# Optimization experiments

Measured on AMD Instinct MI355X. Metric: run time of the kernel, lower is better.

Reference implementation:

```python
import jax, jax.numpy as jnp
import numpy as np

MAX_REL = 127  # default max_relative_position of NEZHA-style RelativePositionsEncoding


def rel_pos_encoding(L, d):
    """Clipped relative-distance sinusoidal encoding, shape [L, L, d]."""
    vocab = 2 * MAX_REL + 1
    pos = np.arange(vocab, dtype=np.float32)[:, None]
    i = np.arange(d)
    div = np.power(10000.0, (2 * (i // 2)) / d).astype(np.float32)
    ang = pos / div
    table = np.where(i % 2 == 0, np.sin(ang), np.cos(ang)).astype(np.float32)  # [vocab, d]
    dist = np.clip(np.arange(L)[None, :] - np.arange(L)[:, None], -MAX_REL, MAX_REL) + MAX_REL
    return jnp.asarray(table[dist])  # [L, L, d]


def setup_inputs() -> dict:
    key = jax.random.key(0)
    ks = jax.random.split(key, 5)
    B, L, H, C = 2, 256, 256, 5
    return {
        "hidden_state": jax.random.normal(ks[0], (B, L, H), dtype=jnp.float32),
        "mask": jnp.ones((B, L), dtype=jnp.int32),
        "Wh_w": jax.random.normal(ks[1], (4 * H, H), dtype=jnp.float32) * 0.02,
        "Wh_b": jax.random.normal(ks[2], (H,), dtype=jnp.float32) * 0.02,
        "Wo_w": jax.random.normal(ks[3], (H, C), dtype=jnp.float32) * 0.02,
        "Wo_b": jax.random.normal(ks[4], (C,), dtype=jnp.float32) * 0.02,
    }


def reference(hidden_state, mask, Wh_w, Wh_b, Wo_w, Wo_b):
    B, L, H = hidden_state.shape
    # Decompose Wh over the concat [end, start, end-start, end*start]:
    # Wh(cat) = end@(We+Wd) + start@(Ws-Wd) + (end*start)@Wm + rel@Wh + b  (exact, linearity)
    We, Ws, Wd, Wm = jnp.split(Wh_w, 4, axis=0)  # each [H, H]
    rel = rel_pos_encoding(L, 4 * H)                        # [L, L, 4H]
    rel_term = jnp.einsum('ijk,kh->ijh', rel, Wh_w)         # [L, L, H]
    a = hidden_state @ (We + Wd)                            # end-index contribution  [B, L, H]
    b = hidden_state @ (Ws - Wd)                            # start-index contribution [B, L, H]
    prod = hidden_state[:, :, None, :] * hidden_state[:, None, :, :]  # [B, L, L, H]
    pre = a[:, :, None, :] + b[:, None, :, :] + prod @ Wm + rel_term[None] + Wh_b
    hij = jnp.tanh(pre)                                     # [B, L, L, H]
    logits = hij @ Wo_w + Wo_b                              # [B, L, L, C]
    logits = jnp.transpose(logits, (0, 3, 1, 2))            # [B, C, L, L]
    m = mask.astype(bool)
    bad = (~m[:, None, :, None]) | (~m[:, None, None, :])
    logits = jnp.where(bad, -jnp.inf, logits)
    tri = jnp.tril(jnp.ones((L, L), logits.dtype), -1) * 1e12
    return logits - tri
```

## Files before the change

kernel.cpp:

```cpp
#include <hip/hip_runtime.h>
#include <math.h>

typedef _Float16 half8 __attribute__((ext_vector_type(8)));
typedef _Float16 half4v __attribute__((ext_vector_type(4)));
typedef float floatx4 __attribute__((ext_vector_type(4)));

union U16 { uint4 u; half8 h; };

__global__ __launch_bounds__(256) void k_prep1(
    const float* __restrict__ hs, const float* __restrict__ Wh,
    const float* __restrict__ Wo,
    float* __restrict__ Rp, float* __restrict__ ap, float* __restrict__ bp,
    uint4* __restrict__ WmT2, uint4* __restrict__ WoPk)
{
  __shared__ __align__(16) char pool[32768];
  int bid = blockIdx.x, tid = threadIdx.x;

  if (bid < 512) {
    float (*tbl)[4] = (float(*)[4])pool;
    int dg = bid >> 3, kq = bid & 7, d0 = dg * 4, k0 = kq * 128;
    for (int idx = tid; idx < 512; idx += 256) {
      int t = idx >> 2, dl = idx & 3;
      int k = k0 + t;
      float e = (float)(k & ~1) * (1.0f / 1024.f);
      float div = powf(10000.f, e);
      float ang = (float)(d0 + dl) / div;
      tbl[t][dl] = (k & 1) ? cosf(ang) : sinf(ang);
    }
    __syncthreads();
    int h = tid;
    float acc[4] = {0, 0, 0, 0};
    for (int kk = 0; kk < 128; ++kk) {
      float wv = Wh[(k0 + kk) * 256 + h];
      float4 tr = *(const float4*)&tbl[kk][0];
      acc[0] = fmaf(tr.x, wv, acc[0]);
      acc[1] = fmaf(tr.y, wv, acc[1]);
      acc[2] = fmaf(tr.z, wv, acc[2]);
      acc[3] = fmaf(tr.w, wv, acc[3]);
    }
#pragma unroll
    for (int dl = 0; dl < 4; ++dl)
      Rp[kq * 65536 + (d0 + dl) * 256 + h] = acc[dl];

  } else if (bid < 1024) {
    float (*xs)[4] = (float(*)[4])pool;
    int g = bid - 512, rg = g >> 2, kq = g & 3;
    int r0 = rg * 4, k0 = kq * 64;
    {
      int r = tid >> 6, kk = tid & 63;
      xs[kk][r] = hs[(size_t)(r0 + r) * 256 + k0 + kk];
    }
    __syncthreads();
    int h = tid;
    float aa[4] = {0, 0, 0, 0}, bb[4] = {0, 0, 0, 0};
    for (int kk = 0; kk < 64; ++kk) {
      int k = k0 + kk;
      float we = Wh[k * 256 + h];
      float wsv = Wh[(256 + k) * 256 + h];
      float wd = Wh[(512 + k) * 256 + h];
      float wA = we + wd, wB = wsv - wd;
      float4 xr = *(const float4*)&xs[kk][0];
      aa[0] = fmaf(xr.x, wA, aa[0]);  bb[0] = fmaf(xr.x, wB, bb[0]);
      aa[1] = fmaf(xr.y, wA, aa[1]);  bb[1] = fmaf(xr.y, wB, bb[1]);
      aa[2] = fmaf(xr.z, wA, aa[2]);  bb[2] = fmaf(xr.z, wB, bb[2]);
      aa[3] = fmaf(xr.w, wA, aa[3]);  bb[3] = fmaf(xr.w, wB, bb[3]);
    }
#pragma unroll
    for (int r = 0; r < 4; ++r) {
      ap[kq * 131072 + (r0 + r) * 256 + h] = aa[r];
      bp[kq * 131072 + (r0 + r) * 256 + h] = bb[r];
    }

  } else if (bid < 1028) {
    _Float16 (*T)[256] = (_Float16(*)[256])pool;
    int q = bid - 1024;
    for (int idx = tid; idx < 16384; idx += 256) {
      int k = idx >> 8, h = idx & 255;
      T[k][h] = (_Float16)Wh[(768 + q * 64 + k) * 256 + h];
    }
    __syncthreads();
    for (int gi = tid; gi < 2048; gi += 256) {
      int kbl = gi >> 8, h = gi & 255;
      U16 v;
#pragma unroll
      for (int e = 0; e < 8; ++e) v.h[e] = T[kbl * 8 + e][h];
      WmT2[(q * 8 + kbl) * 256 + h] = v.u;
    }

  } else {
    for (int gi = tid; gi < 512; gi += 256) {
      int kb = gi >> 4, c = gi & 15;
      U16 v;
#pragma unroll
      for (int e = 0; e < 8; ++e)
        v.h[e] = (c < 5) ? (_Float16)Wo[(kb * 8 + e) * 5 + c] : (_Float16)0.f;
      WoPk[gi] = v.u;
    }
  }
}

__global__ __launch_bounds__(256) void k_prep2(
    const float* __restrict__ Rp, const float* __restrict__ ap,
    const float* __restrict__ bp,
    float* __restrict__ R, float* __restrict__ a, float* __restrict__ bv)
{
  int bid = blockIdx.x, h = threadIdx.x;
  if (bid < 255) {
    int d = bid;
    float s = 0.f;
#pragma unroll
    for (int kq = 0; kq < 8; ++kq) s += Rp[kq * 65536 + d * 256 + h];
    R[d * 256 + h] = s;
  } else {
    int r0 = (bid - 255) * 2;
#pragma unroll
    for (int rr = 0; rr < 2; ++rr) {
      int r = r0 + rr;
      float sa = 0.f, sb = 0.f;
#pragma unroll
      for (int kq = 0; kq < 4; ++kq) {
        sa += ap[kq * 131072 + r * 256 + h];
        sb += bp[kq * 131072 + r * 256 + h];
      }
      a[r * 256 + h] = sa;
      bv[r * 256 + h] = sb;
    }
  }
}

__global__ __launch_bounds__(256, 4) void k_main(
    const float* __restrict__ hs, const int* __restrict__ mask,
    const float* __restrict__ R, const float* __restrict__ a,
    const float* __restrict__ bvec, const float* __restrict__ Whb,
    const uint4* __restrict__ WmT2, const uint4* __restrict__ WoPk,
    const float* __restrict__ Wob, float* __restrict__ out)
{
  __shared__ __align__(16) char smem[34304];
  _Float16 (*As)[264] = (_Float16(*)[264])smem;
  float (*stg)[268] = (float(*)[268])smem;

  int bid = blockIdx.x, tid = threadIdx.x;
  int jt = bid & 3, i = (bid >> 2) & 255, b = bid >> 10;
  int j0 = jt * 64;
  int lane = tid & 63, w = tid >> 6;
  int c16 = lane & 15, quad = lane >> 4;
  const float* hsb = hs + (size_t)b * 65536;

  float av[4];
#pragma unroll
  for (int ht2 = 0; ht2 < 4; ++ht2) {
    int hp = 64 * w + 16 * ht2 + c16;
    av[ht2] = a[((size_t)(b * 256 + i)) * 256 + hp] + Whb[hp];
  }

  floatx4 acc[4][4];
#pragma unroll
  for (int hf = 0; hf < 2; ++hf) {
    int jbase = j0 + hf * 32;
#pragma unroll
    for (int it = 0; it < 8; ++it) {
      int idx = it * 256 + tid;
      int row = idx >> 6;
      int c4 = (idx & 63) << 2;
      int jg = jbase + row;
      int dd = jg - i;
      dd = dd < -127 ? -127 : (dd > 127 ? 127 : dd);
      dd += 127;
      float4 bb = *(const float4*)(bvec + ((size_t)(b * 256 + jg)) * 256 + c4);
      float4 rr = *(const float4*)(R + (size_t)dd * 256 + c4);
      float4 s;
      s.x = bb.x + rr.x; s.y = bb.y + rr.y;
      s.z = bb.z + rr.z; s.w = bb.w + rr.w;
      *(float4*)&stg[row][c4] = s;
    }
    __syncthreads();
#pragma unroll
    for (int jj = 0; jj < 2; ++jj) {
      int jt2 = hf * 2 + jj;
#pragma unroll
      for (int r = 0; r < 4; ++r) {
        int jl32 = jj * 16 + quad * 4 + r;
#pragma unroll
        for (int ht2 = 0; ht2 < 4; ++ht2)
          acc[jt2][ht2][r] = av[ht2] + stg[jl32][64 * w + 16 * ht2 + c16];
      }
    }
    __syncthreads();
  }

  {
    int k8 = (tid & 31) * 8;
    float4 xi0 = *(const float4*)(hsb + i * 256 + k8);
    float4 xi1 = *(const float4*)(hsb + i * 256 + k8 + 4);
    int j = tid >> 5;
#pragma unroll
    for (int s = 0; s < 8; ++s, j += 8) {
      float4 xj0 = *(const float4*)(hsb + (j0 + j) * 256 + k8);
      float4 xj1 = *(const float4*)(hsb + (j0 + j) * 256 + k8 + 4);
      half8 p = {(_Float16)(xi0.x * xj0.x), (_Float16)(xi0.y * xj0.y),
                 (_Float16)(xi0.z * xj0.z), (_Float16)(xi0.w * xj0.w),
                 (_Float16)(xi1.x * xj1.x), (_Float16)(xi1.y * xj1.y),
                 (_Float16)(xi1.z * xj1.z), (_Float16)(xi1.w * xj1.w)};
      *(half8*)(&As[j][k8]) = p;
    }
  }
  __syncthreads();

  {
    int hbase = 64 * w + c16;
    U16 bgA[4], bgB[4];
#pragma unroll
    for (int ht2 = 0; ht2 < 4; ++ht2)
      bgA[ht2].u = WmT2[quad * 256 + hbase + 16 * ht2];
#pragma unroll 1
    for (int it2 = 0; it2 < 4; ++it2) {
      int itE = it2 * 2, itO = itE + 1;
#pragma unroll
      for (int ht2 = 0; ht2 < 4; ++ht2)
        bgB[ht2].u = WmT2[(itO * 4 + quad) * 256 + hbase + 16 * ht2];
      {
        half8 af[4];
#pragma unroll
        for (int jt2 = 0; jt2 < 4; ++jt2)
          af[jt2] = *(const half8*)(&As[jt2 * 16 + c16][itE * 32 + quad * 8]);
#pragma unroll
        for (int jt2 = 0; jt2 < 4; ++jt2)
#pragma unroll
          for (int ht2 = 0; ht2 < 4; ++ht2)
            acc[jt2][ht2] = __builtin_amdgcn_mfma_f32_16x16x32_f16(
                af[jt2], bgA[ht2].h, acc[jt2][ht2], 0, 0, 0);
      }
      if (it2 < 3) {
#pragma unroll
        for (int ht2 = 0; ht2 < 4; ++ht2)
          bgA[ht2].u = WmT2[((itE + 2) * 4 + quad) * 256 + hbase + 16 * ht2];
      }
      {
        half8 af[4];
#pragma unroll
        for (int jt2 = 0; jt2 < 4; ++jt2)
          af[jt2] = *(const half8*)(&As[jt2 * 16 + c16][itO * 32 + quad * 8]);
#pragma unroll
        for (int jt2 = 0; jt2 < 4; ++jt2)
#pragma unroll
          for (int ht2 = 0; ht2 < 4; ++ht2)
            acc[jt2][ht2] = __builtin_amdgcn_mfma_f32_16x16x32_f16(
                af[jt2], bgB[ht2].h, acc[jt2][ht2], 0, 0, 0);
      }
    }
  }

  __syncthreads();

#pragma unroll
  for (int jt2 = 0; jt2 < 4; ++jt2) {
#pragma unroll
    for (int ht2 = 0; ht2 < 4; ++ht2) {
      int hp = 64 * w + 16 * ht2 + c16;
#pragma unroll
      for (int r = 0; r < 4; ++r) {
        int jl = jt2 * 16 + quad * 4 + r;
        float x = acc[jt2][ht2][r];
        float e = __expf(2.f * x);
        float t = fmaf(-2.f, __builtin_amdgcn_rcpf(e + 1.f), 1.f);
        As[jl][hp] = (_Float16)t;
      }
    }
  }
  __syncthreads();

  {
    U16 wog[8];
#pragma unroll
    for (int s = 0; s < 8; ++s) wog[s].u = WoPk[(s * 4 + quad) * 16 + c16];
    floatx4 accE = {0.f, 0.f, 0.f, 0.f};
#pragma unroll
    for (int s = 0; s < 8; ++s) {
      half8 ae = *(const half8*)(&As[16 * w + c16][s * 32 + quad * 8]);
      accE = __builtin_amdgcn_mfma_f32_16x16x32_f16(ae, wog[s].h, accE, 0, 0, 0);
    }
    const int* mb = mask + b * 256;
    int mi = mb[i];
    int jg0 = j0 + 16 * w + quad * 4;
    int mj[4];
    *(int4*)mj = *(const int4*)(mb + jg0);
    float wob = (c16 < 5) ? Wob[c16] : 0.f;
    float4 v;
#pragma unroll
    for (int r = 0; r < 4; ++r) {
      int jg = jg0 + r;
      float x = accE[r] + wob;
      if (!(mi && mj[r])) x = -INFINITY;
      if (jg < i) x -= 1e12f;
      ((float*)&v)[r] = x;
    }
    if (c16 < 5)
      *(float4*)(&out[(((size_t)b * 5 + c16) * 256 + i) * 256 + jg0]) = v;
  }
}

extern "C" void kernel_launch(void* const* d_in, const int* in_sizes, int n_in,
                              void* d_out, int out_size, void* d_ws, size_t ws_size,
                              hipStream_t stream) {
  const float* hs   = (const float*)d_in[0];
  const int*   mask = (const int*)d_in[1];
  const float* Wh_w = (const float*)d_in[2];
  const float* Wh_b = (const float*)d_in[3];
  const float* Wo_w = (const float*)d_in[4];
  const float* Wo_b = (const float*)d_in[5];

  char* ws = (char*)d_ws;
  float* R    = (float*)(ws + 0);
  float* a    = (float*)(ws + 262144);
  float* bv   = (float*)(ws + 786432);
  uint4* WmT2 = (uint4*)(ws + 1310720);
  uint4* WoPk = (uint4*)(ws + 1441792);
  float* Rp   = (float*)(ws + 1449984);
  float* ap   = (float*)(ws + 3547136);
  float* bp   = (float*)(ws + 5644288);

  k_prep1<<<1029, 256, 0, stream>>>(hs, Wh_w, Wo_w, Rp, ap, bp, WmT2, WoPk);
  k_prep2<<<511, 256, 0, stream>>>(Rp, ap, bp, R, a, bv);
  k_main<<<2048, 256, 0, stream>>>(hs, mask, R, a, bv, Wh_b, WmT2, WoPk, Wo_b,
                                   (float*)d_out);
}
```

Before: 115.4 us.

## Fuse partial-sum reduction into prep kernel via last-block atomic counters

Removes the separate k_prep2 reduction kernel. Each group of partial-product blocks in the prep kernel now bumps an atomic counter after a threadfence, and the last block to finish sums the partials into R, a and bv. This is meant to cut one kernel launch and the serialization gap between the prep stages. In exchange it adds a hipMemsetAsync to zero the counters on every call, plus atomics and fences in the prep kernel.

Result: slower. 238.8 us (+106.9%).

```diff
diff --git a/kernel.cpp b/kernel.cpp
--- a/kernel.cpp
+++ b/kernel.cpp
@@ -7,13 +7,15 @@
 
 union U16 { uint4 u; half8 h; };
 
-__global__ __launch_bounds__(256) void k_prep1(
+__global__ __launch_bounds__(256) void k_prep(
     const float* __restrict__ hs, const float* __restrict__ Wh,
     const float* __restrict__ Wo,
     float* __restrict__ Rp, float* __restrict__ ap, float* __restrict__ bp,
-    uint4* __restrict__ WmT2, uint4* __restrict__ WoPk)
+    float* __restrict__ R, float* __restrict__ a, float* __restrict__ bv,
+    uint4* __restrict__ WmT2, uint4* __restrict__ WoPk, int* __restrict__ cnt)
 {
   __shared__ __align__(16) char pool[32768];
+  __shared__ int lastFlag;
   int bid = blockIdx.x, tid = threadIdx.x;
 
   if (bid < 512) {
@@ -41,6 +43,22 @@
 #pragma unroll
     for (int dl = 0; dl < 4; ++dl)
       Rp[kq * 65536 + (d0 + dl) * 256 + h] = acc[dl];
+
+    __threadfence();
+    __syncthreads();
+    if (tid == 0) lastFlag = (atomicAdd(&cnt[dg], 1) == 7);
+    __syncthreads();
+    if (lastFlag) {
+      __threadfence();
+#pragma unroll
+      for (int dl = 0; dl < 4; ++dl) {
+        int d = d0 + dl;
+        float s = 0.f;
+#pragma unroll
+        for (int q = 0; q < 8; ++q) s += Rp[q * 65536 + d * 256 + h];
+        R[d * 256 + h] = s;
+      }
+    }
 
   } else if (bid < 1024) {
     float (*xs)[4] = (float(*)[4])pool;
@@ -71,6 +89,25 @@
       bp[kq * 131072 + (r0 + r) * 256 + h] = bb[r];
     }
 
+    __threadfence();
+    __syncthreads();
+    if (tid == 0) lastFlag = (atomicAdd(&cnt[64 + rg], 1) == 3);
+    __syncthreads();
+    if (lastFlag) {
+      __threadfence();
+#pragma unroll
+      for (int r = 0; r < 4; ++r) {
+        float sa = 0.f, sb = 0.f;
+#pragma unroll
+        for (int q = 0; q < 4; ++q) {
+          sa += ap[q * 131072 + (r0 + r) * 256 + h];
+          sb += bp[q * 131072 + (r0 + r) * 256 + h];
+        }
+        a[(size_t)(r0 + r) * 256 + h] = sa;
+        bv[(size_t)(r0 + r) * 256 + h] = sb;
+      }
+    }
+
   } else if (bid < 1028) {
     _Float16 (*T)[256] = (_Float16(*)[256])pool;
     int q = bid - 1024;
@@ -95,35 +132,6 @@
       for (int e = 0; e < 8; ++e)
         v.h[e] = (c < 5) ? (_Float16)Wo[(kb * 8 + e) * 5 + c] : (_Float16)0.f;
       WoPk[gi] = v.u;
-    }
-  }
-}
-
-__global__ __launch_bounds__(256) void k_prep2(
-    const float* __restrict__ Rp, const float* __restrict__ ap,
-    const float* __restrict__ bp,
-    float* __restrict__ R, float* __restrict__ a, float* __restrict__ bv)
-{
-  int bid = blockIdx.x, h = threadIdx.x;
-  if (bid < 255) {
-    int d = bid;
-    float s = 0.f;
-#pragma unroll
-    for (int kq = 0; kq < 8; ++kq) s += Rp[kq * 65536 + d * 256 + h];
-    R[d * 256 + h] = s;
-  } else {
-    int r0 = (bid - 255) * 2;
-#pragma unroll
-    for (int rr = 0; rr < 2; ++rr) {
-      int r = r0 + rr;
-      float sa = 0.f, sb = 0.f;
-#pragma unroll
-      for (int kq = 0; kq < 4; ++kq) {
-        sa += ap[kq * 131072 + r * 256 + h];
-        sb += bp[kq * 131072 + r * 256 + h];
-      }
-      a[r * 256 + h] = sa;
-      bv[r * 256 + h] = sb;
     }
   }
 }
@@ -318,9 +326,11 @@
   float* Rp   = (float*)(ws + 1449984);
   float* ap   = (float*)(ws + 3547136);
   float* bp   = (float*)(ws + 5644288);
-
-  k_prep1<<<1029, 256, 0, stream>>>(hs, Wh_w, Wo_w, Rp, ap, bp, WmT2, WoPk);
-  k_prep2<<<511, 256, 0, stream>>>(Rp, ap, bp, R, a, bv);
+  int*   cnt  = (int*)(ws + 7741440);
+
+  hipMemsetAsync(cnt, 0, 192 * sizeof(int), stream);
+  k_prep<<<1029, 256, 0, stream>>>(hs, Wh_w, Wo_w, Rp, ap, bp, R, a, bv,
+                                   WmT2, WoPk, cnt);
   k_main<<<2048, 256, 0, stream>>>(hs, mask, R, a, bv, Wh_b, WmT2, WoPk, Wo_b,
                                    (float*)d_out);
 }
```

## Merge the two prep kernels with an in-block split-K reduction in shared memory

Applied to the files above, without the earlier changes.

The two preprocessing kernels become one 512-thread kernel. Each block now splits K across its wavefronts and sums the partial results in shared memory. This removes the second kernel launch and the global round trip for the partial buffers Rp, ap and bp. Weight loads also change to float4 vectors, with each thread producing four h outputs. In exchange the prep launches far fewer blocks (261 instead of 1029), so less parallelism is exposed while the sin/cos table and the matmuls run.

Measured after the change: 113.5 us. About the same (-1.7%).

```diff
diff --git a/kernel.cpp b/kernel.cpp
--- a/kernel.cpp
+++ b/kernel.cpp
@@ -7,79 +7,111 @@
 
 union U16 { uint4 u; half8 h; };
 
-__global__ __launch_bounds__(256) void k_prep1(
+__global__ __launch_bounds__(512) void k_prep(
     const float* __restrict__ hs, const float* __restrict__ Wh,
     const float* __restrict__ Wo,
-    float* __restrict__ Rp, float* __restrict__ ap, float* __restrict__ bp,
+    float* __restrict__ R, float* __restrict__ a, float* __restrict__ bv,
     uint4* __restrict__ WmT2, uint4* __restrict__ WoPk)
 {
   __shared__ __align__(16) char pool[32768];
   int bid = blockIdx.x, tid = threadIdx.x;
-
-  if (bid < 512) {
-    float (*tbl)[4] = (float(*)[4])pool;
-    int dg = bid >> 3, kq = bid & 7, d0 = dg * 4, k0 = kq * 128;
-    for (int idx = tid; idx < 512; idx += 256) {
-      int t = idx >> 2, dl = idx & 3;
-      int k = k0 + t;
+  int w = tid >> 6, lane = tid & 63;
+
+  if (bid < 128) {
+    float (*tbl2)[2] = (float(*)[2])pool;
+    float (*red)[2][256] = (float(*)[2][256])(pool + 8192);
+    int d0 = bid * 2;
+#pragma unroll
+    for (int s = 0; s < 4; ++s) {
+      int idx = s * 512 + tid;
+      int k = idx >> 1, dl = idx & 1;
       float e = (float)(k & ~1) * (1.0f / 1024.f);
       float div = powf(10000.f, e);
       float ang = (float)(d0 + dl) / div;
-      tbl[t][dl] = (k & 1) ? cosf(ang) : sinf(ang);
-    }
-    __syncthreads();
-    int h = tid;
-    float acc[4] = {0, 0, 0, 0};
+      tbl2[k][dl] = (k & 1) ? cosf(ang) : sinf(ang);
+    }
+    __syncthreads();
+    int h0 = lane * 4, k0 = w * 128;
+    floatx4 acc0 = {0.f, 0.f, 0.f, 0.f}, acc1 = {0.f, 0.f, 0.f, 0.f};
     for (int kk = 0; kk < 128; ++kk) {
-      float wv = Wh[(k0 + kk) * 256 + h];
-      float4 tr = *(const float4*)&tbl[kk][0];
-      acc[0] = fmaf(tr.x, wv, acc[0]);
-      acc[1] = fmaf(tr.y, wv, acc[1]);
-      acc[2] = fmaf(tr.z, wv, acc[2]);
-      acc[3] = fmaf(tr.w, wv, acc[3]);
-    }
-#pragma unroll
-    for (int dl = 0; dl < 4; ++dl)
-      Rp[kq * 65536 + (d0 + dl) * 256 + h] = acc[dl];
-
-  } else if (bid < 1024) {
-    float (*xs)[4] = (float(*)[4])pool;
-    int g = bid - 512, rg = g >> 2, kq = g & 3;
-    int r0 = rg * 4, k0 = kq * 64;
+      int k = k0 + kk;
+      float4 wv = *(const float4*)(Wh + (size_t)k * 256 + h0);
+      float t0 = tbl2[k][0], t1 = tbl2[k][1];
+      acc0[0] = fmaf(t0, wv.x, acc0[0]); acc1[0] = fmaf(t1, wv.x, acc1[0]);
+      acc0[1] = fmaf(t0, wv.y, acc0[1]); acc1[1] = fmaf(t1, wv.y, acc1[1]);
+      acc0[2] = fmaf(t0, wv.z, acc0[2]); acc1[2] = fmaf(t1, wv.z, acc1[2]);
+      acc0[3] = fmaf(t0, wv.w, acc0[3]); acc1[3] = fmaf(t1, wv.w, acc1[3]);
+    }
+    *(floatx4*)&red[w][0][h0] = acc0;
+    *(floatx4*)&red[w][1][h0] = acc1;
+    __syncthreads();
     {
-      int r = tid >> 6, kk = tid & 63;
-      xs[kk][r] = hs[(size_t)(r0 + r) * 256 + k0 + kk];
-    }
-    __syncthreads();
-    int h = tid;
-    float aa[4] = {0, 0, 0, 0}, bb[4] = {0, 0, 0, 0};
+      int h = tid & 255, dl = tid >> 8;
+      float s = 0.f;
+#pragma unroll
+      for (int q = 0; q < 8; ++q) s += red[q][dl][h];
+      R[(size_t)(d0 + dl) * 256 + h] = s;
+    }
+
+  } else if (bid < 256) {
+    float (*redA)[4][256] = (float(*)[4][256])pool;
+    float (*redB)[4][256] = (float(*)[4][256])(pool + 16384);
+    int r0 = (bid - 128) * 4;
+    int kq = w & 3, rp = w >> 2;
+    int k0 = kq * 64, h0 = lane * 4;
+    int rA = r0 + rp * 2, rB = rA + 1;
+    floatx4 aa0 = {0.f,0.f,0.f,0.f}, bb0 = {0.f,0.f,0.f,0.f};
+    floatx4 aa1 = {0.f,0.f,0.f,0.f}, bb1 = {0.f,0.f,0.f,0.f};
     for (int kk = 0; kk < 64; ++kk) {
       int k = k0 + kk;
-      float we = Wh[k * 256 + h];
-      float wsv = Wh[(256 + k) * 256 + h];
-      float wd = Wh[(512 + k) * 256 + h];
-      float wA = we + wd, wB = wsv - wd;
-      float4 xr = *(const float4*)&xs[kk][0];
-      aa[0] = fmaf(xr.x, wA, aa[0]);  bb[0] = fmaf(xr.x, wB, bb[0]);
-      aa[1] = fmaf(xr.y, wA, aa[1]);  bb[1] = fmaf(xr.y, wB, bb[1]);
-      aa[2] = fmaf(xr.z, wA, aa[2]);  bb[2] = fmaf(xr.z, wB, bb[2]);
-      aa[3] = fmaf(xr.w, wA, aa[3]);  bb[3] = fmaf(xr.w, wB, bb[3]);
-    }
-#pragma unroll
-    for (int r = 0; r < 4; ++r) {
-      ap[kq * 131072 + (r0 + r) * 256 + h] = aa[r];
-      bp[kq * 131072 + (r0 + r) * 256 + h] = bb[r];
-    }
-
-  } else if (bid < 1028) {
+      float4 we = *(const float4*)(Wh + (size_t)k * 256 + h0);
+      float4 ws = *(const float4*)(Wh + (size_t)(256 + k) * 256 + h0);
+      float4 wd = *(const float4*)(Wh + (size_t)(512 + k) * 256 + h0);
+      float wA0 = we.x + wd.x, wB0 = ws.x - wd.x;
+      float wA1 = we.y + wd.y, wB1 = ws.y - wd.y;
+      float wA2 = we.z + wd.z, wB2 = ws.z - wd.z;
+      float wA3 = we.w + wd.w, wB3 = ws.w - wd.w;
+      float x0 = hs[(size_t)rA * 256 + k];
+      float x1 = hs[(size_t)rB * 256 + k];
+      aa0[0] = fmaf(x0, wA0, aa0[0]); bb0[0] = fmaf(x0, wB0, bb0[0]);
+      aa0[1] = fmaf(x0, wA1, aa0[1]); bb0[1] = fmaf(x0, wB1, bb0[1]);
+      aa0[2] = fmaf(x0, wA2, aa0[2]); bb0[2] = fmaf(x0, wB2, bb0[2]);
+      aa0[3] = fmaf(x0, wA3, aa0[3]); bb0[3] = fmaf(x0, wB3, bb0[3]);
+      aa1[0] = fmaf(x1, wA0, aa1[0]); bb1[0] = fmaf(x1, wB0, bb1[0]);
+      aa1[1] = fmaf(x1, wA1, aa1[1]); bb1[1] = fmaf(x1, wB1, bb1[1]);
+      aa1[2] = fmaf(x1, wA2, aa1[2]); bb1[2] = fmaf(x1, wB2, bb1[2]);
+      aa1[3] = fmaf(x1, wA3, aa1[3]); bb1[3] = fmaf(x1, wB3, bb1[3]);
+    }
+    *(floatx4*)&redA[kq][rp * 2 + 0][h0] = aa0;
+    *(floatx4*)&redA[kq][rp * 2 + 1][h0] = aa1;
+    *(floatx4*)&redB[kq][rp * 2 + 0][h0] = bb0;
+    *(floatx4*)&redB[kq][rp * 2 + 1][h0] = bb1;
+    __syncthreads();
+    {
+      int h = tid & 255, rr = tid >> 8;
+#pragma unroll
+      for (int j = 0; j < 2; ++j) {
+        int row = rr * 2 + j;
+        float sa = 0.f, sb = 0.f;
+#pragma unroll
+        for (int q = 0; q < 4; ++q) {
+          sa += redA[q][row][h];
+          sb += redB[q][row][h];
+        }
+        a[(size_t)(r0 + row) * 256 + h] = sa;
+        bv[(size_t)(r0 + row) * 256 + h] = sb;
+      }
+    }
+
+  } else if (bid < 260) {
     _Float16 (*T)[256] = (_Float16(*)[256])pool;
-    int q = bid - 1024;
-    for (int idx = tid; idx < 16384; idx += 256) {
+    int q = bid - 256;
+    for (int idx = tid; idx < 16384; idx += 512) {
       int k = idx >> 8, h = idx & 255;
       T[k][h] = (_Float16)Wh[(768 + q * 64 + k) * 256 + h];
     }
     __syncthreads();
-    for (int gi = tid; gi < 2048; gi += 256) {
+    for (int gi = tid; gi < 2048; gi += 512) {
       int kbl = gi >> 8, h = gi & 255;
       U16 v;
 #pragma unroll
@@ -88,42 +120,13 @@
     }
 
   } else {
-    for (int gi = tid; gi < 512; gi += 256) {
-      int kb = gi >> 4, c = gi & 15;
+    if (tid < 512) {
+      int kb = tid >> 4, c = tid & 15;
       U16 v;
 #pragma unroll
       for (int e = 0; e < 8; ++e)
         v.h[e] = (c < 5) ? (_Float16)Wo[(kb * 8 + e) * 5 + c] : (_Float16)0.f;
-      WoPk[gi] = v.u;
-    }
-  }
-}
-
-__global__ __launch_bounds__(256) void k_prep2(
-    const float* __restrict__ Rp, const float* __restrict__ ap,
-    const float* __restrict__ bp,
-    float* __restrict__ R, float* __restrict__ a, float* __restrict__ bv)
-{
-  int bid = blockIdx.x, h = threadIdx.x;
-  if (bid < 255) {
-    int d = bid;
-    float s = 0.f;
-#pragma unroll
-    for (int kq = 0; kq < 8; ++kq) s += Rp[kq * 65536 + d * 256 + h];
-    R[d * 256 + h] = s;
-  } else {
-    int r0 = (bid - 255) * 2;
-#pragma unroll
-    for (int rr = 0; rr < 2; ++rr) {
-      int r = r0 + rr;
-      float sa = 0.f, sb = 0.f;
-#pragma unroll
-      for (int kq = 0; kq < 4; ++kq) {
-        sa += ap[kq * 131072 + r * 256 + h];
-        sb += bp[kq * 131072 + r * 256 + h];
-      }
-      a[r * 256 + h] = sa;
-      bv[r * 256 + h] = sb;
+      WoPk[tid] = v.u;
     }
   }
 }
@@ -315,12 +318,8 @@
   float* bv   = (float*)(ws + 786432);
   uint4* WmT2 = (uint4*)(ws + 1310720);
   uint4* WoPk = (uint4*)(ws + 1441792);
-  float* Rp   = (float*)(ws + 1449984);
-  float* ap   = (float*)(ws + 3547136);
-  float* bp   = (float*)(ws + 5644288);
-
-  k_prep1<<<1029, 256, 0, stream>>>(hs, Wh_w, Wo_w, Rp, ap, bp, WmT2, WoPk);
-  k_prep2<<<511, 256, 0, stream>>>(Rp, ap, bp, R, a, bv);
+
+  k_prep<<<261, 512, 0, stream>>>(hs, Wh_w, Wo_w, R, a, bv, WmT2, WoPk);
   k_main<<<2048, 256, 0, stream>>>(hs, mask, R, a, bv, Wh_b, WmT2, WoPk, Wo_b,
                                    (float*)d_out);
 }
```
